# Optimization experiments

Hardware: AMD Instinct MI355X
Metric: run time of the kernel (lower is better)

Reference implementation:

```python
import jax, jax.numpy as jnp
import numpy as np

RATIOS = (0.5, 1.0, 2.0)
SCALES = (8.0, 16.0, 32.0)
FEAT_STRIDE = 16
BASE_SIZE = 16.0
NMS_THRESH = 0.7
N_PRE = 6000   # pre-NMS top-k (eval-mode ProposalCreator default)
N_POST = 300   # post-NMS proposals per image (eval-mode default)
MIN_SIZE = 16.0
SCALE = 1.0


def generate_anchor_base():
    ab = np.zeros((len(RATIOS) * len(SCALES), 4), np.float32)
    for i, r in enumerate(RATIOS):
        for j, s in enumerate(SCALES):
            h = BASE_SIZE * s * np.sqrt(r)
            w = BASE_SIZE * s * np.sqrt(1.0 / r)
            ab[i * len(SCALES) + j] = [-h / 2.0, -w / 2.0, h / 2.0, w / 2.0]
    return jnp.asarray(ab)


def enumerate_shifted_anchor(anchor_base, feat_stride, H, W):
    sy = jnp.arange(H, dtype=jnp.float32) * feat_stride
    sx = jnp.arange(W, dtype=jnp.float32) * feat_stride
    sx, sy = jnp.meshgrid(sx, sy)  # row-major over (y, x), matching torch permute order
    shift = jnp.stack([sy.ravel(), sx.ravel(), sy.ravel(), sx.ravel()], axis=1)  # [K,4]
    anchors = anchor_base[None, :, :] + shift[:, None, :]  # [K, A, 4]
    return anchors.reshape(-1, 4)


def loc2bbox(anchor, loc):
    # boxes in (y1, x1, y2, x2) format
    h = anchor[:, 2] - anchor[:, 0]
    w = anchor[:, 3] - anchor[:, 1]
    cy = anchor[:, 0] + 0.5 * h
    cx = anchor[:, 1] + 0.5 * w
    dy, dx, dh, dw = loc[:, 0], loc[:, 1], loc[:, 2], loc[:, 3]
    cy = cy + dy * h
    cx = cx + dx * w
    h = h * jnp.exp(dh)
    w = w * jnp.exp(dw)
    return jnp.stack([cy - 0.5 * h, cx - 0.5 * w, cy + 0.5 * h, cx + 0.5 * w], axis=1)


def nms_fixed(boxes, scores):
    # boxes [N_PRE,4] sorted desc by scores; greedy NMS emitting N_POST picks (padded)
    area = (boxes[:, 2] - boxes[:, 0]) * (boxes[:, 3] - boxes[:, 1])

    def step(sc, _):
        i = jnp.argmax(sc)
        v = sc[i] > -jnp.inf
        b = boxes[i]
        yy1 = jnp.maximum(boxes[:, 0], b[0])
        xx1 = jnp.maximum(boxes[:, 1], b[1])
        yy2 = jnp.minimum(boxes[:, 2], b[2])
        xx2 = jnp.minimum(boxes[:, 3], b[3])
        inter = jnp.maximum(yy2 - yy1, 0.0) * jnp.maximum(xx2 - xx1, 0.0)
        iou = inter / (area + area[i] - inter + 1e-9)
        sc = jnp.where((iou > NMS_THRESH) & v, -jnp.inf, sc)
        sc = sc.at[i].set(-jnp.inf)
        return sc, (i, v)

    _, (idx, valid) = jax.lax.scan(step, scores, None, length=N_POST)
    return jnp.where(valid[:, None], boxes[idx], 0.0)  # [N_POST, 4]


def proposal_one(loc, score, anchor, img_h, img_w):
    roi = loc2bbox(anchor, loc)
    roi = jnp.stack([
        jnp.clip(roi[:, 0], 0.0, img_h), jnp.clip(roi[:, 1], 0.0, img_w),
        jnp.clip(roi[:, 2], 0.0, img_h), jnp.clip(roi[:, 3], 0.0, img_w)], axis=1)
    hs = roi[:, 2] - roi[:, 0]
    ws = roi[:, 3] - roi[:, 1]
    min_size = MIN_SIZE * SCALE
    valid = (hs >= min_size) & (ws >= min_size)
    s = jnp.where(valid, score, -jnp.inf)
    top_s, top_i = jax.lax.top_k(s, N_PRE)
    return nms_fixed(roi[top_i], top_s)


def setup_inputs() -> dict:
    key = jax.random.key(0)
    ks = jax.random.split(key, 4)
    B, C, H, W = 8, 512, 64, 64
    A = 9
    return {
        "x": jax.random.normal(ks[0], (B, C, H, W), jnp.float32),
        "conv_w": jax.random.normal(ks[1], (C, C, 3, 3), jnp.float32) * 0.01,
        "conv_b": jnp.zeros((C,), jnp.float32),
        "loc_w": jax.random.normal(ks[2], (A * 4, C, 1, 1), jnp.float32) * 0.01,
        "loc_b": jnp.zeros((A * 4,), jnp.float32),
        "cls_w": jax.random.normal(ks[3], (A * 2, C, 1, 1), jnp.float32) * 0.01,
        "cls_b": jnp.zeros((A * 2,), jnp.float32),
        "img_h": 1024,
        "img_w": 1024,
    }


def reference(x, conv_w, conv_b, loc_w, loc_b, cls_w, cls_b, img_h, img_w):
    dn = ("NCHW", "OIHW", "NCHW")
    h = jax.lax.conv_general_dilated(x, conv_w, (1, 1), "SAME", dimension_numbers=dn)
    h = jax.nn.relu(h + conv_b[None, :, None, None])
    cls = jax.nn.sigmoid(
        jax.lax.conv_general_dilated(h, cls_w, (1, 1), "VALID", dimension_numbers=dn)
        + cls_b[None, :, None, None])
    loc = (jax.lax.conv_general_dilated(h, loc_w, (1, 1), "VALID", dimension_numbers=dn)
           + loc_b[None, :, None, None])
    B, _, H, W = h.shape
    anchor = enumerate_shifted_anchor(generate_anchor_base(), FEAT_STRIDE, H, W)
    pred_locations = loc.transpose(0, 2, 3, 1).reshape(B, -1, 4)          # [B, HWA, 4]
    cls_hw = cls.transpose(0, 2, 3, 1)                                     # [B, H, W, 2A]
    objectness = cls_hw.reshape(B, H, W, -1, 2)[..., 1].reshape(B, -1)     # [B, HWA]
    pred_cls_scores = cls_hw.reshape(B, -1, 2)                             # [B, HWA, 2]
    fh = jnp.float32(img_h)
    fw = jnp.float32(img_w)
    rois = jax.vmap(lambda l, s: proposal_one(l, s, anchor, fh, fw))(pred_locations, objectness)
    rois = rois.reshape(B * N_POST, 4)
    roi_indices = jnp.repeat(jnp.arange(B, dtype=jnp.int64 if jax.config.jax_enable_x64 else jnp.int32), N_POST)
    return pred_cls_scores, pred_locations, rois, roi_indices
```

## Files before the change

### kernel.cpp

```cpp
#include <hip/hip_runtime.h>
#include <cstdint>
#include <cmath>


__global__ __launch_bounds__(256) void k_conv3x3(
        const float* __restrict__ x, const float* __restrict__ w,
        const float* __restrict__ bias, float* __restrict__ hout) {
    __shared__ __align__(16) float xs[8][4][68];
    __shared__ __align__(16) float wl[8][9][64];
    const int ypair = blockIdx.x;
    const int co0 = blockIdx.y * 64;
    const int b = blockIdx.z;
    const int t = threadIdx.x;
    const int xq = t & 7;
    const int coq = (t >> 3) & 15;
    const int yy = t >> 7;
    const int y0 = ypair * 2;

    float acc[4][8];
#pragma unroll
    for (int c = 0; c < 4; ++c)
#pragma unroll
        for (int i = 0; i < 8; ++i) acc[c][i] = 0.f;

    const int co_s = t >> 2, q_s = t & 3;

    for (int ci0 = 0; ci0 < 512; ci0 += 8) {
        __syncthreads();
        for (int idx = t; idx < 2112; idx += 256) {
            int ci = idx / 264;
            int rem = idx - ci * 264;
            int ry = rem / 66;
            int xx = rem - ry * 66 - 1;
            int gy = y0 - 1 + ry;
            float v = 0.f;
            if (gy >= 0 && gy < 64 && xx >= 0 && xx < 64)
                v = x[(((size_t)b * 512 + ci0 + ci) * 64 + gy) * 64 + xx];
            xs[ci][ry][xx + 1] = v;
        }
        {
            const float* wp = w + ((size_t)(co0 + co_s) * 512 + ci0) * 9 + q_s * 18;
#pragma unroll
            for (int j = 0; j < 18; ++j) {
                int f = q_s * 18 + j;
                int ci = f / 9, kk = f - ci * 9;
                wl[ci][kk][co_s] = wp[j];
            }
        }
        __syncthreads();
#pragma unroll
        for (int ci = 0; ci < 8; ++ci) {
#pragma unroll
            for (int ky = 0; ky < 3; ++ky) {
                const float* xr = &xs[ci][yy + ky][xq * 8];
                float4 v0 = *reinterpret_cast<const float4*>(xr);
                float4 v1 = *reinterpret_cast<const float4*>(xr + 4);
                float xv[10];
                xv[0] = v0.x; xv[1] = v0.y; xv[2] = v0.z; xv[3] = v0.w;
                xv[4] = v1.x; xv[5] = v1.y; xv[6] = v1.z; xv[7] = v1.w;
                xv[8] = xr[8]; xv[9] = xr[9];
#pragma unroll
                for (int kx = 0; kx < 3; ++kx) {
                    const float4 wv = *reinterpret_cast<const float4*>(&wl[ci][ky * 3 + kx][coq * 4]);
#pragma unroll
                    for (int i = 0; i < 8; ++i) {
                        float xvv = xv[i + kx];
                        acc[0][i] += wv.x * xvv;
                        acc[1][i] += wv.y * xvv;
                        acc[2][i] += wv.z * xvv;
                        acc[3][i] += wv.w * xvv;
                    }
                }
            }
        }
    }
    const int y = y0 + yy;
#pragma unroll
    for (int c = 0; c < 4; ++c) {
        const int co = co0 + coq * 4 + c;
        const float bv = bias[co];
        float* op = hout + (((size_t)b * 512 + co) * 64 + y) * 64 + xq * 8;
#pragma unroll
        for (int i = 0; i < 8; ++i) {
            float v = acc[c][i] + bv;
            op[i] = v > 0.f ? v : 0.f;
        }
    }
}

__global__ __launch_bounds__(256) void k_head(
        const float* __restrict__ h,
        const float* __restrict__ cls_w, const float* __restrict__ cls_b,
        const float* __restrict__ loc_w, const float* __restrict__ loc_b,
        const int* __restrict__ img_h_p, const int* __restrict__ img_w_p,
        float* __restrict__ out_cls, float* __restrict__ out_loc,
        float* __restrict__ boxes, float* __restrict__ scores) {
    const int tg = blockIdx.x * 256 + threadIdx.x;
    const int b = tg >> 12;
    const int pos = tg & 4095;
    const int y = pos >> 6, xc = pos & 63;
    float accC[18], accL[36];
#pragma unroll
    for (int o = 0; o < 18; ++o) accC[o] = 0.f;
#pragma unroll
    for (int o = 0; o < 36; ++o) accL[o] = 0.f;
    const float* hp = h + (size_t)b * 2097152 + pos;
#pragma unroll 4
    for (int ci = 0; ci < 512; ++ci) {
        const float hv = hp[(size_t)ci * 4096];
#pragma unroll
        for (int o = 0; o < 18; ++o) accC[o] += cls_w[o * 512 + ci] * hv;
#pragma unroll
        for (int o = 0; o < 36; ++o) accL[o] += loc_w[o * 512 + ci] * hv;
    }
    const float fh = (float)(*img_h_p);
    const float fw = (float)(*img_w_p);
    {
        const size_t obase = (size_t)b * 73728 + (size_t)pos * 18;
#pragma unroll
        for (int o = 0; o < 18; ++o) {
            accC[o] += cls_b[o];
            out_cls[obase + o] = 1.f / (1.f + expf(-accC[o]));
        }
    }
    {
        const size_t lbase = (size_t)b * 147456 + (size_t)pos * 36;
#pragma unroll
        for (int o = 0; o < 36; ++o) {
            accL[o] += loc_b[o];
            out_loc[lbase + o] = accL[o];
        }
    }
    const float sy = (float)(y * 16), sx = (float)(xc * 16);
    const double RR[3] = {0.5, 1.0, 2.0};
    const double SS[3] = {8.0, 16.0, 32.0};
#pragma unroll
    for (int a = 0; a < 9; ++a) {
        const double r = RR[a / 3], s = SS[a % 3];
        const double hd = 16.0 * s * sqrt(r);
        const double wd = 16.0 * s * sqrt(1.0 / r);
        const float ab0 = (float)(-hd / 2.0), ab1 = (float)(-wd / 2.0);
        const float ab2 = (float)(hd / 2.0), ab3 = (float)(wd / 2.0);
        const float a0 = ab0 + sy, a1 = ab1 + sx, a2 = ab2 + sy, a3 = ab3 + sx;
        float hh = a2 - a0, ww = a3 - a1;
        float cy = a0 + 0.5f * hh, cx = a1 + 0.5f * ww;
        const float dy = accL[a * 4 + 0], dx = accL[a * 4 + 1];
        const float dh = accL[a * 4 + 2], dw = accL[a * 4 + 3];
        cy = cy + dy * hh;
        cx = cx + dx * ww;
        hh = hh * expf(dh);
        ww = ww * expf(dw);
        float y1 = cy - 0.5f * hh, x1 = cx - 0.5f * ww;
        float y2 = cy + 0.5f * hh, x2 = cx + 0.5f * ww;
        y1 = fminf(fmaxf(y1, 0.f), fh); x1 = fminf(fmaxf(x1, 0.f), fw);
        y2 = fminf(fmaxf(y2, 0.f), fh); x2 = fminf(fmaxf(x2, 0.f), fw);
        const bool valid = ((y2 - y1) >= 16.f) && ((x2 - x1) >= 16.f);
        const float sc = 1.f / (1.f + expf(-accC[a * 2 + 1]));
        const int n = pos * 9 + a;
        float* bp = boxes + ((size_t)b * 36864 + n) * 4;
        bp[0] = y1; bp[1] = x1; bp[2] = y2; bp[3] = x2;
        scores[(size_t)b * 36864 + n] = valid ? sc : -INFINITY;
    }
}

__device__ __forceinline__ unsigned fmap(float f) {
    unsigned bits = __float_as_uint(f);
    return ((int)bits < 0) ? ~bits : (bits | 0x80000000u);
}

__global__ __launch_bounds__(1024) void k_select(
        const float* __restrict__ scores, unsigned* __restrict__ sel) {
    __shared__ unsigned hist[256];
    __shared__ unsigned tieL[1024];
    __shared__ unsigned sh_pref, sh_k, sh_cg, sh_ct;
    const int b = blockIdx.x;
    const int t = threadIdx.x;
    const float* sp = scores + (size_t)b * 36864;
    unsigned pref = 0;
    unsigned k = 6000;
    for (int p = 3; p >= 0; --p) {
        if (t < 256) hist[t] = 0;
        __syncthreads();
        for (int i = t; i < 36864; i += 1024) {
            unsigned u = fmap(sp[i]);
            bool match = (p == 3) || ((u >> ((p + 1) * 8)) == (pref >> ((p + 1) * 8)));
            if (match) atomicAdd(&hist[(u >> (p * 8)) & 255], 1u);
        }
        __syncthreads();
        if (t == 0) {
            unsigned c = 0;
            int bsel = 0;
            for (int bin = 255; bin >= 0; --bin) {
                unsigned c2 = c + hist[bin];
                if (c2 >= k) { bsel = bin; k = k - c; break; }
                c = c2;
            }
            pref |= ((unsigned)bsel) << (p * 8);
            sh_pref = pref; sh_k = k;
        }
        __syncthreads();
        pref = sh_pref; k = sh_k;
        __syncthreads();
    }
    if (t == 0) { sh_cg = 0; sh_ct = 0; }
    __syncthreads();
    const unsigned uthr = pref;
    for (int i = t; i < 36864; i += 1024) {
        unsigned u = fmap(sp[i]);
        if (u > uthr) {
            unsigned posn = atomicAdd(&sh_cg, 1u);
            sel[(size_t)b * 6000 + posn] = (unsigned)i;
        } else if (u == uthr) {
            unsigned tp = atomicAdd(&sh_ct, 1u);
            if (tp < 1024) tieL[tp] = (unsigned)i;
        }
    }
    __syncthreads();
    const unsigned G = sh_cg;
    const unsigned T = sh_ct;
    const unsigned need = k;
    const unsigned Tc = T < 1024u ? T : 1024u;
    if ((unsigned)t >= Tc) tieL[t] = 0xFFFFFFFFu;
    __syncthreads();
    if (need > 0) {
        if (T > 1) {
            for (int kk = 2; kk <= 1024; kk <<= 1) {
                for (int j = kk >> 1; j > 0; j >>= 1) {
                    int ixj = t ^ j;
                    if (ixj > t) {
                        unsigned va = tieL[t], vb = tieL[ixj];
                        bool up = ((t & kk) == 0);
                        if (up ? (va > vb) : (va < vb)) { tieL[t] = vb; tieL[ixj] = va; }
                    }
                    __syncthreads();
                }
            }
        }
        if ((unsigned)t < need) sel[(size_t)b * 6000 + G + t] = tieL[t];
    }
}

__global__ __launch_bounds__(1024) void k_nms(
        const float* __restrict__ boxes, const float* __restrict__ scores,
        const unsigned* __restrict__ sel,
        float* __restrict__ rois, float* __restrict__ roi_idx) {
    __shared__ unsigned long long warr[16];
    __shared__ unsigned long long winK;
    const int b = blockIdx.x;
    const int t = threadIdx.x;
    const unsigned UNEG = 0x007FFFFFu;
    float bx[6][4];
    unsigned long long key[6];
#pragma unroll
    for (int j = 0; j < 6; ++j) {
        int s = t + j * 1024;
        if (s < 6000) {
            unsigned idx = sel[(size_t)b * 6000 + s];
            const float* bp = boxes + ((size_t)b * 36864 + idx) * 4;
            bx[j][0] = bp[0]; bx[j][1] = bp[1]; bx[j][2] = bp[2]; bx[j][3] = bp[3];
            unsigned u = fmap(scores[(size_t)b * 36864 + idx]);
            key[j] = ((unsigned long long)u << 32) | (unsigned)(~idx);
        } else {
            key[j] = 0ull;
            bx[j][0] = bx[j][1] = bx[j][2] = bx[j][3] = 0.f;
        }
    }
    const int lane = t & 63;
    const int wid = t >> 6;
    float* orow = rois + (size_t)b * 300 * 4;
    for (int k = 0; k < 300; ++k) {
        unsigned long long m = key[0];
#pragma unroll
        for (int j = 1; j < 6; ++j) m = key[j] > m ? key[j] : m;
#pragma unroll
        for (int d = 32; d > 0; d >>= 1) {
            unsigned long long o = __shfl_xor(m, d, 64);
            if (o > m) m = o;
        }
        if (lane == 0) warr[wid] = m;
        __syncthreads();
        if (t == 0) {
            unsigned long long wv = warr[0];
#pragma unroll
            for (int i = 1; i < 16; ++i) if (warr[i] > wv) wv = warr[i];
            winK = wv;
        }
        __syncthreads();
        const unsigned long long wk = winK;
        const unsigned uhi = (unsigned)(wk >> 32);
        if (uhi > UNEG) {
            const unsigned widx = ~(unsigned)wk;
            const float* bp = boxes + ((size_t)b * 36864 + widx) * 4;
            const float py1 = bp[0], px1 = bp[1], py2 = bp[2], px2 = bp[3];
            const float parea = (py2 - py1) * (px2 - px1);
            if (t == 0) {
                orow[k * 4 + 0] = py1; orow[k * 4 + 1] = px1;
                orow[k * 4 + 2] = py2; orow[k * 4 + 3] = px2;
                roi_idx[b * 300 + k] = (float)b;
            }
#pragma unroll
            for (int j = 0; j < 6; ++j) {
                if ((unsigned)(key[j] >> 32) > UNEG) {
                    float yy1 = fmaxf(bx[j][0], py1);
                    float xx1 = fmaxf(bx[j][1], px1);
                    float yy2 = fminf(bx[j][2], py2);
                    float xx2 = fminf(bx[j][3], px2);
                    float inter = fmaxf(yy2 - yy1, 0.f) * fmaxf(xx2 - xx1, 0.f);
                    float area = (bx[j][2] - bx[j][0]) * (bx[j][3] - bx[j][1]);
                    float iou = inter / (area + parea - inter + 1e-9f);
                    if (iou > 0.7f)
                        key[j] = ((unsigned long long)UNEG << 32) | (key[j] & 0xFFFFFFFFull);
                }
            }
        } else {
            if (t == 0) {
                orow[k * 4 + 0] = 0.f; orow[k * 4 + 1] = 0.f;
                orow[k * 4 + 2] = 0.f; orow[k * 4 + 3] = 0.f;
                roi_idx[b * 300 + k] = (float)b;
            }
        }
        __syncthreads();
    }
}

extern "C" void kernel_launch(void* const* d_in, const int* in_sizes, int n_in,
                              void* d_out, int out_size, void* d_ws, size_t ws_size,
                              hipStream_t stream) {
    (void)in_sizes; (void)n_in; (void)out_size; (void)ws_size;
    const float* x      = (const float*)d_in[0];
    const float* conv_w = (const float*)d_in[1];
    const float* conv_b = (const float*)d_in[2];
    const float* loc_w  = (const float*)d_in[3];
    const float* loc_b  = (const float*)d_in[4];
    const float* cls_w  = (const float*)d_in[5];
    const float* cls_b  = (const float*)d_in[6];
    const int* img_h    = (const int*)d_in[7];
    const int* img_w    = (const int*)d_in[8];

    char* ws = (char*)d_ws;
    float*    h      = (float*)(ws + 0);
    float*    boxes  = (float*)(ws + 67108864);
    float*    scores = (float*)(ws + 71827456);
    unsigned* sel    = (unsigned*)(ws + 73007104);

    float* out      = (float*)d_out;
    float* out_cls  = out;
    float* out_loc  = out + 589824;
    float* rois     = out + 1769472;
    float* ridx     = out + 1779072;

    k_conv3x3<<<dim3(32, 8, 8), 256, 0, stream>>>(x, conv_w, conv_b, h);
    k_head<<<dim3(128), 256, 0, stream>>>(h, cls_w, cls_b, loc_w, loc_b,
                                          img_h, img_w, out_cls, out_loc, boxes, scores);
    k_select<<<dim3(8), 1024, 0, stream>>>(scores, sel);
    k_nms<<<dim3(8), 1024, 0, stream>>>(boxes, scores, sel, rois, ridx);
}
```

Measured before the change: 3.419 ms.

## Enlarge conv register tile, load input via direct global-to-LDS, aggregate select atomics

```diff
diff --git a/kernel.cpp b/kernel.cpp
--- a/kernel.cpp
+++ b/kernel.cpp
@@ -3,48 +3,67 @@
 #include <cmath>
 
 
-__global__ __launch_bounds__(256) void k_conv3x3(
+#define AS1U(p) ((const __attribute__((address_space(1))) unsigned int*)(p))
+#define AS3U(p) ((__attribute__((address_space(3))) unsigned int*)(p))
+
+__global__ __launch_bounds__(256, 4) void k_conv3x3(
         const float* __restrict__ x, const float* __restrict__ w,
-        const float* __restrict__ bias, float* __restrict__ hout) {
-    __shared__ __align__(16) float xs[8][4][68];
-    __shared__ __align__(16) float wl[8][9][64];
-    const int ypair = blockIdx.x;
+        const float* __restrict__ bias, const float* __restrict__ zeropad,
+        float* __restrict__ hout) {
+    __shared__ __align__(16) float xs[8][6][68];
+    __shared__ __align__(16) float wl[8][9][68];
+
+    const int ytile = blockIdx.x;
     const int co0 = blockIdx.y * 64;
     const int b = blockIdx.z;
     const int t = threadIdx.x;
     const int xq = t & 7;
-    const int coq = (t >> 3) & 15;
-    const int yy = t >> 7;
-    const int y0 = ypair * 2;
-
-    float acc[4][8];
-#pragma unroll
-    for (int c = 0; c < 4; ++c)
+    const int coq = (t >> 3) & 7;
+    const int yy = t >> 6;
+    const int lane = t & 63;
+    const int y0 = ytile * 4;
+
+    if (t < 48) { int ci = t / 6, ry = t % 6; xs[ci][ry][0] = 0.f; xs[ci][ry][65] = 0.f; }
+
+    float acc[8][8];
+#pragma unroll
+    for (int c = 0; c < 8; ++c)
 #pragma unroll
         for (int i = 0; i < 8; ++i) acc[c][i] = 0.f;
 
-    const int co_s = t >> 2, q_s = t & 3;
+    const int co_s = t >> 2, qs = t & 3;
+    const float* wsrc = w + (size_t)(co0 + co_s) * 4608 + qs * 18;
+    float* wrow = &wl[0][0][0] + (size_t)(2 * qs) * 9 * 68 + co_s;
+
+    const int gy0 = y0 - 1;
+    const float* xb = x + ((size_t)b * 512) * 4096;
 
     for (int ci0 = 0; ci0 < 512; ci0 += 8) {
         __syncthreads();
-        for (int idx = t; idx < 2112; idx += 256) {
-            int ci = idx / 264;
-            int rem = idx - ci * 264;
-            int ry = rem / 66;
-            int xx = rem - ry * 66 - 1;
-            int gy = y0 - 1 + ry;
-            float v = 0.f;
-            if (gy >= 0 && gy < 64 && xx >= 0 && xx < 64)
-                v = x[(((size_t)b * 512 + ci0 + ci) * 64 + gy) * 64 + xx];
-            xs[ci][ry][xx + 1] = v;
-        }
         {
-            const float* wp = w + ((size_t)(co0 + co_s) * 512 + ci0) * 9 + q_s * 18;
+#pragma unroll
+            for (int j = 0; j < 12; ++j) {
+                const int ci = 2 * yy + (j >= 6 ? 1 : 0);
+                const int ry = (j >= 6) ? (j - 6) : j;
+                const int gy = gy0 + ry;
+                const float* src = (gy >= 0 && gy < 64)
+                    ? xb + ((size_t)(ci0 + ci) * 64 + gy) * 64 + lane
+                    : zeropad + lane;
+                __builtin_amdgcn_global_load_lds(AS1U(src), AS3U(&xs[ci][ry][1]), 4, 0, 0);
+            }
+        }
+        {
+            const float2* wp2 = (const float2*)(wsrc + (size_t)ci0 * 9);
+            float wv[18];
+#pragma unroll
+            for (int j2 = 0; j2 < 9; ++j2) {
+                float2 f = wp2[j2];
+                wv[2 * j2] = f.x; wv[2 * j2 + 1] = f.y;
+            }
 #pragma unroll
             for (int j = 0; j < 18; ++j) {
-                int f = q_s * 18 + j;
-                int ci = f / 9, kk = f - ci * 9;
-                wl[ci][kk][co_s] = wp[j];
+                const int k = (j < 9) ? j : (j - 9);
+                wrow[((j >= 9) ? 9 * 68 : 0) + k * 68] = wv[j];
             }
         }
         __syncthreads();
@@ -53,22 +72,24 @@
 #pragma unroll
             for (int ky = 0; ky < 3; ++ky) {
                 const float* xr = &xs[ci][yy + ky][xq * 8];
-                float4 v0 = *reinterpret_cast<const float4*>(xr);
-                float4 v1 = *reinterpret_cast<const float4*>(xr + 4);
-                float xv[10];
-                xv[0] = v0.x; xv[1] = v0.y; xv[2] = v0.z; xv[3] = v0.w;
-                xv[4] = v1.x; xv[5] = v1.y; xv[6] = v1.z; xv[7] = v1.w;
-                xv[8] = xr[8]; xv[9] = xr[9];
+                const float4 a0 = *(const float4*)(xr);
+                const float4 a1 = *(const float4*)(xr + 4);
+                const float2 a2 = *(const float2*)(xr + 8);
+                float xw[10];
+                xw[0] = a0.x; xw[1] = a0.y; xw[2] = a0.z; xw[3] = a0.w;
+                xw[4] = a1.x; xw[5] = a1.y; xw[6] = a1.z; xw[7] = a1.w;
+                xw[8] = a2.x; xw[9] = a2.y;
 #pragma unroll
                 for (int kx = 0; kx < 3; ++kx) {
-                    const float4 wv = *reinterpret_cast<const float4*>(&wl[ci][ky * 3 + kx][coq * 4]);
+                    const float4 w0 = *(const float4*)&wl[ci][ky * 3 + kx][coq * 8];
+                    const float4 w1 = *(const float4*)&wl[ci][ky * 3 + kx][coq * 8 + 4];
 #pragma unroll
                     for (int i = 0; i < 8; ++i) {
-                        float xvv = xv[i + kx];
-                        acc[0][i] += wv.x * xvv;
-                        acc[1][i] += wv.y * xvv;
-                        acc[2][i] += wv.z * xvv;
-                        acc[3][i] += wv.w * xvv;
+                        const float xv = xw[i + kx];
+                        acc[0][i] += w0.x * xv; acc[1][i] += w0.y * xv;
+                        acc[2][i] += w0.z * xv; acc[3][i] += w0.w * xv;
+                        acc[4][i] += w1.x * xv; acc[5][i] += w1.y * xv;
+                        acc[6][i] += w1.z * xv; acc[7][i] += w1.w * xv;
                     }
                 }
             }
@@ -76,15 +97,17 @@
     }
     const int y = y0 + yy;
 #pragma unroll
-    for (int c = 0; c < 4; ++c) {
-        const int co = co0 + coq * 4 + c;
+    for (int c = 0; c < 8; ++c) {
+        const int co = co0 + coq * 8 + c;
         const float bv = bias[co];
         float* op = hout + (((size_t)b * 512 + co) * 64 + y) * 64 + xq * 8;
-#pragma unroll
-        for (int i = 0; i < 8; ++i) {
-            float v = acc[c][i] + bv;
-            op[i] = v > 0.f ? v : 0.f;
-        }
+        float4 o0, o1;
+        o0.x = fmaxf(acc[c][0] + bv, 0.f); o0.y = fmaxf(acc[c][1] + bv, 0.f);
+        o0.z = fmaxf(acc[c][2] + bv, 0.f); o0.w = fmaxf(acc[c][3] + bv, 0.f);
+        o1.x = fmaxf(acc[c][4] + bv, 0.f); o1.y = fmaxf(acc[c][5] + bv, 0.f);
+        o1.z = fmaxf(acc[c][6] + bv, 0.f); o1.w = fmaxf(acc[c][7] + bv, 0.f);
+        *(float4*)(op) = o0;
+        *(float4*)(op + 4) = o1;
     }
 }
 
@@ -175,16 +198,27 @@
     __shared__ unsigned sh_pref, sh_k, sh_cg, sh_ct;
     const int b = blockIdx.x;
     const int t = threadIdx.x;
+    const int lane = t & 63;
+    const unsigned long long lmlt = (1ull << lane) - 1ull;
     const float* sp = scores + (size_t)b * 36864;
     unsigned pref = 0;
     unsigned k = 6000;
     for (int p = 3; p >= 0; --p) {
         if (t < 256) hist[t] = 0;
         __syncthreads();
+        const int sh = p * 8;
         for (int i = t; i < 36864; i += 1024) {
             unsigned u = fmap(sp[i]);
-            bool match = (p == 3) || ((u >> ((p + 1) * 8)) == (pref >> ((p + 1) * 8)));
-            if (match) atomicAdd(&hist[(u >> (p * 8)) & 255], 1u);
+            bool match = (p == 3) || ((u >> (sh + 8)) == (pref >> (sh + 8)));
+            unsigned bin = (u >> sh) & 255u;
+            unsigned long long act = __ballot(match);
+            while (act) {
+                int lead = __ffsll((unsigned long long)act) - 1;
+                unsigned lbin = __shfl(bin, lead, 64);
+                unsigned long long same = __ballot(match && (bin == lbin));
+                if (lane == lead) atomicAdd(&hist[lbin], (unsigned)__popcll(same));
+                act &= ~same;
+            }
         }
         __syncthreads();
         if (t == 0) {
@@ -195,7 +229,7 @@
                 if (c2 >= k) { bsel = bin; k = k - c; break; }
                 c = c2;
             }
-            pref |= ((unsigned)bsel) << (p * 8);
+            pref |= ((unsigned)bsel) << sh;
             sh_pref = pref; sh_k = k;
         }
         __syncthreads();
@@ -207,12 +241,26 @@
     const unsigned uthr = pref;
     for (int i = t; i < 36864; i += 1024) {
         unsigned u = fmap(sp[i]);
-        if (u > uthr) {
-            unsigned posn = atomicAdd(&sh_cg, 1u);
-            sel[(size_t)b * 6000 + posn] = (unsigned)i;
-        } else if (u == uthr) {
-            unsigned tp = atomicAdd(&sh_ct, 1u);
-            if (tp < 1024) tieL[tp] = (unsigned)i;
+        const bool g = (u > uthr);
+        const bool e = (u == uthr);
+        unsigned long long bg = __ballot(g);
+        if (bg) {
+            int lead = __ffsll((unsigned long long)bg) - 1;
+            unsigned basev = 0;
+            if (lane == lead) basev = atomicAdd(&sh_cg, (unsigned)__popcll(bg));
+            basev = __shfl(basev, lead, 64);
+            if (g) sel[(size_t)b * 6000 + basev + (unsigned)__popcll(bg & lmlt)] = (unsigned)i;
+        }
+        unsigned long long be = __ballot(e);
+        if (be) {
+            int lead = __ffsll((unsigned long long)be) - 1;
+            unsigned baset = 0;
+            if (lane == lead) baset = atomicAdd(&sh_ct, (unsigned)__popcll(be));
+            baset = __shfl(baset, lead, 64);
+            if (e) {
+                unsigned tp = baset + (unsigned)__popcll(be & lmlt);
+                if (tp < 1024) tieL[tp] = (unsigned)i;
+            }
         }
     }
     __syncthreads();
@@ -342,6 +390,7 @@
     float*    boxes  = (float*)(ws + 67108864);
     float*    scores = (float*)(ws + 71827456);
     unsigned* sel    = (unsigned*)(ws + 73007104);
+    float*    zp     = (float*)(ws + 73199104);
 
     float* out      = (float*)d_out;
     float* out_cls  = out;
@@ -349,7 +398,8 @@
     float* rois     = out + 1769472;
     float* ridx     = out + 1779072;
 
-    k_conv3x3<<<dim3(32, 8, 8), 256, 0, stream>>>(x, conv_w, conv_b, h);
+    hipMemsetAsync(zp, 0, 256, stream);
+    k_conv3x3<<<dim3(16, 8, 8), 256, 0, stream>>>(x, conv_w, conv_b, zp, h);
     k_head<<<dim3(128), 256, 0, stream>>>(h, cls_w, cls_b, loc_w, loc_b,
                                           img_h, img_w, out_cls, out_loc, boxes, scores);
     k_select<<<dim3(8), 1024, 0, stream>>>(scores, sel);
```

Measured after the change: 4.421 ms. 29.3% more time.
